# Optimization experiments

Hardware: AMD Instinct MI355X
Metric: run time of the kernel (lower is better)

## Reference

```python
import jax, jax.numpy as jnp
import numpy as np

N, E = 50000, 400000
D_NODE, D_EDGE = 128, 16
MSG_DIM, OUT_DIM = 128, 128
H_MSG, H_AGGR, H_UP = 256, 128, 256


def _dense(key, fin, fout):
    # xavier_uniform-scale gaussian init (exact distribution irrelevant for correctness)
    scale = jnp.sqrt(2.0 / (fin + fout)).astype(jnp.float32)
    w = jax.random.normal(key, (fin, fout), jnp.float32) * scale
    b = jnp.zeros((fout,), jnp.float32)
    return w, b


def setup_inputs() -> dict:
    key = jax.random.key(0)
    ks = jax.random.split(key, 13)
    nodes = jax.random.normal(ks[0], (N, D_NODE), jnp.float32)
    edges = jax.random.normal(ks[1], (E, D_EDGE), jnp.float32)
    senders = jax.random.randint(ks[2], (E,), 0, N, jnp.int32)
    receivers = jax.random.randint(ks[3], (E,), 0, N, jnp.int32)
    msg_in = D_EDGE + 2 * D_NODE
    msg_w1, msg_b1 = _dense(ks[4], msg_in, H_MSG)
    msg_w2, msg_b2 = _dense(ks[5], H_MSG, H_MSG)
    msg_w3, msg_b3 = _dense(ks[6], H_MSG, MSG_DIM)
    ag_w1, ag_b1 = _dense(ks[7], MSG_DIM, H_AGGR)
    ag_w2, ag_b2 = _dense(ks[8], H_AGGR, H_AGGR)
    ag_w3, ag_b3 = _dense(ks[9], H_AGGR, 1)
    up_w1, up_b1 = _dense(ks[10], D_NODE + MSG_DIM, H_UP)
    up_w2, up_b2 = _dense(ks[11], H_UP, H_UP)
    up_w3, up_b3 = _dense(ks[12], H_UP, OUT_DIM)
    return dict(nodes=nodes, edges=edges, senders=senders, receivers=receivers,
                msg_w1=msg_w1, msg_b1=msg_b1, msg_w2=msg_w2, msg_b2=msg_b2,
                msg_w3=msg_w3, msg_b3=msg_b3,
                ag_w1=ag_w1, ag_b1=ag_b1, ag_w2=ag_w2, ag_b2=ag_b2,
                ag_w3=ag_w3, ag_b3=ag_b3,
                up_w1=up_w1, up_b1=up_b1, up_w2=up_w2, up_b2=up_b2,
                up_w3=up_w3, up_b3=up_b3)


def reference(nodes, edges, senders, receivers,
              msg_w1, msg_b1, msg_w2, msg_b2, msg_w3, msg_b3,
              ag_w1, ag_b1, ag_w2, ag_b2, ag_w3, ag_b3,
              up_w1, up_b1, up_w2, up_b2, up_w3, up_b3):
    n = nodes.shape[0]
    # message_fn: concat(edge, sender, receiver) -> MLP(256,256) -> Dense(msg_dim)
    feats = jnp.concatenate([edges, nodes[senders], nodes[receivers]], axis=-1)  # [E, d_e+2d_n]
    h = jax.nn.relu(feats @ msg_w1 + msg_b1)      # relu after first hidden only (act_final=False)
    h = h @ msg_w2 + msg_b2
    msgs = h @ msg_w3 + msg_b3                    # [E, msg_dim]
    # aggregate_fn: gate MLP(128,128) -> Dense(1) -> segment_softmax over receivers
    g = jax.nn.relu(msgs @ ag_w1 + ag_b1)
    g = g @ ag_w2 + ag_b2
    gate = (g @ ag_w3 + ag_b3)[:, 0]              # [E]
    seg_max = jax.ops.segment_max(gate, receivers, num_segments=n)  # [N]
    w = jnp.exp(gate - seg_max[receivers])
    denom = jax.ops.segment_sum(w, receivers, num_segments=n)       # [N]
    attn = w / denom[receivers]                   # [E]
    aggr = jax.ops.segment_sum(attn[:, None] * msgs, receivers, num_segments=n)  # [N, msg_dim]
    # update_fn: concat(node, aggr) -> MLP(256,256) -> Dense(out_dim)
    u = jnp.concatenate([nodes, aggr], axis=-1)
    h = jax.nn.relu(u @ up_w1 + up_b1)
    h = h @ up_w2 + up_b2
    out = h @ up_w3 + up_b3                       # [N, out_dim]
    return out
```

## Files before the change

### kernel.cpp

```cpp
#include <hip/hip_runtime.h>
#include <stdint.h>


typedef _Float16 h16;
typedef _Float16 half8  __attribute__((ext_vector_type(8)));
typedef _Float16 h16x2  __attribute__((ext_vector_type(2)));
typedef float    f32x16 __attribute__((ext_vector_type(16)));
typedef unsigned u32x4  __attribute__((ext_vector_type(4)));

__device__ __forceinline__ f32x16 MFMA(half8 a, half8 b, f32x16 c) {
  return __builtin_amdgcn_mfma_f32_32x32x16_f16(a, b, c, 0, 0, 0);
}

__device__ __forceinline__ void lane_swap(unsigned &a, unsigned &b) {
  asm volatile("v_permlane32_swap_b32 %0, %1" : "+v"(a), "+v"(b));
}

__device__ __forceinline__ unsigned ordf(float f) {
  unsigned b = __float_as_uint(f);
  return (b & 0x80000000u) ? ~b : (b | 0x80000000u);
}
__device__ __forceinline__ float ordinv(unsigned u) {
  return __uint_as_float((u & 0x80000000u) ? (u ^ 0x80000000u) : ~u);
}

template<int MFA, int WAVES>
__device__ __forceinline__ void stage_tile(h16* dst, const h16* wT, int K, int kt, int tid) {
  int wv = tid >> 6, lane = tid & 63;
  static_assert((MFA * 2) % WAVES == 0, "tile chunks must divide evenly");
#pragma unroll
  for (int it = 0; it < (MFA * 2) / WAVES; ++it) {
    int slotbase = it * (WAVES * 64) + wv * 64;
    int s = slotbase + lane;
    int row = s >> 2, x = s & 3;
    int c = x ^ ((row >> 1) & 3);
    const h16* src = wT + (size_t)row * K + kt * 32 + c * 8;
    h16* d = dst + slotbase * 8;
    __builtin_amdgcn_global_load_lds((const __attribute__((address_space(1))) unsigned*)src,
                                     (__attribute__((address_space(3))) unsigned*)d, 16, 0, 0);
  }
}

__device__ __forceinline__ half8 ldsA(const h16* buf, int mf, int ksl, int lane) {
  int r31 = lane & 31, g = lane >> 5;
  int c = (2 * ksl + g) ^ ((r31 >> 1) & 3);
  return *(const half8*)(buf + mf * 1024 + r31 * 32 + c * 8);
}

template<bool RELU>
__device__ __forceinline__ void pack_frag(unsigned* hr, const f32x16 a, const float* bias, int g) {
#pragma unroll
  for (int j = 0; j < 8; ++j) {
    int m = 2 * (j & 1) + 8 * (j >> 1) + 4 * g;
    float x = a[2 * j]     + bias[m];
    float y = a[2 * j + 1] + bias[m + 1];
    if (RELU) { x = fmaxf(x, 0.f); y = fmaxf(y, 0.f); }
    auto p = __builtin_amdgcn_cvt_pkrtz(x, y);
    hr[j] = __builtin_bit_cast(unsigned, p);
  }
}

__device__ __forceinline__ half8 buildB(unsigned* hr, int ksl) {
  unsigned v0 = hr[4 * ksl + 0], v1 = hr[4 * ksl + 1];
  unsigned u0 = hr[4 * ksl + 2], u1 = hr[4 * ksl + 3];
  lane_swap(v0, u0);
  lane_swap(v1, u1);
  u32x4 t = {v0, v1, u0, u1};
  return __builtin_bit_cast(half8, t);
}

template<int MFA, int KT, int GB, int NMFA, int WAVES>
__device__ __forceinline__ void gemm_hregB(f32x16* acc, unsigned (*hreg)[8],
    const h16* wT, int K, const h16* nW, int nK,
    h16 (*wbuf)[8192], int tid, int lane) {
#pragma unroll
  for (int kt = 0; kt < KT; ++kt) {
    __syncthreads();
    if (kt + 1 < KT)  stage_tile<MFA, WAVES>(wbuf[(GB + kt + 1) & 1], wT, K, kt + 1, tid);
    else if (nW)      stage_tile<NMFA, WAVES>(wbuf[(GB + kt + 1) & 1], nW, nK, 0, tid);
    const h16* rb = wbuf[(GB + kt) & 1];
    __builtin_amdgcn_s_setprio(1);
#pragma unroll
    for (int ksl = 0; ksl < 2; ++ksl) {
      half8 b = buildB(hreg[kt], ksl);
#pragma unroll
      for (int mf = 0; mf < MFA; ++mf)
        acc[mf] = MFMA(ldsA(rb, mf, ksl, lane), b, acc[mf]);
    }
    __builtin_amdgcn_s_setprio(0);
  }
}

__global__ __launch_bounds__(256, 2) void k_edge(
    const h16* __restrict__ nodes_h, const h16* __restrict__ edges_h,
    const int* __restrict__ senders, const int* __restrict__ receivers,
    const int* __restrict__ perm,
    const h16* __restrict__ w1t, const h16* __restrict__ w2t, const h16* __restrict__ w3t,
    const h16* __restrict__ a1t, const h16* __restrict__ a2t,
    const float* __restrict__ b1, const float* __restrict__ b2, const float* __restrict__ b3,
    const float* __restrict__ ab1, const float* __restrict__ ab2,
    const float* __restrict__ ag3, const float* __restrict__ ab3,
    h16* __restrict__ msgs_h, float* __restrict__ gate, unsigned* __restrict__ segmax, int E)
{
  __shared__ h16 wbuf[2][8192];
  __shared__ float sb[1025];

  int tid = threadIdx.x, lane = tid & 63, wv = tid >> 6;
  int g = lane >> 5, c31 = lane & 31;

  sb[tid] = b1[tid];
  sb[256 + tid] = b2[tid];
  if (tid < 128) {
    sb[512 + tid] = b3[tid];
    sb[640 + tid] = ab1[tid];
    sb[768 + tid] = ab2[tid];
    sb[896 + tid] = ag3[tid];
  }
  if (tid == 0) sb[1024] = ab3[0];

  int e = blockIdx.x * 128 + wv * 32 + c31;
  bool ev = (e < E);
  int ec = ev ? e : (E - 1);
  int se = senders[ec], re = receivers[ec];
  int pidx = perm[ec];
  const h16* pe = edges_h + (size_t)ec * 16;
  const h16* ps = nodes_h + (size_t)se * 128;
  const h16* pr = nodes_h + (size_t)re * 128;

  stage_tile<8, 4>(wbuf[0], w1t, 288, 0, tid);

  auto loadB1 = [&](int ks) -> half8 {
    if (ks >= 17) { half8 z = {}; return z; }
    const h16* base = (ks == 0) ? pe : (ks < 9) ? (ps + 16 * ks - 16) : (pr + 16 * ks - 144);
    return *(const half8*)(base + 8 * g);
  };

  f32x16 acc1[8];
#pragma unroll
  for (int i = 0; i < 8; ++i) acc1[i] = f32x16{};
  half8 bq0 = loadB1(0), bq1 = loadB1(1);
#pragma unroll
  for (int kt = 0; kt < 9; ++kt) {
    __syncthreads();
    if (kt < 8) stage_tile<8, 4>(wbuf[(kt + 1) & 1], w1t, 288, kt + 1, tid);
    else        stage_tile<8, 4>(wbuf[1], w2t, 256, 0, tid);
    half8 n0 = {}, n1 = {};
    if (kt < 8) { n0 = loadB1(2 * kt + 2); n1 = loadB1(2 * kt + 3); }
    const h16* rb = wbuf[kt & 1];
    __builtin_amdgcn_s_setprio(1);
#pragma unroll
    for (int mf = 0; mf < 8; ++mf) acc1[mf] = MFMA(ldsA(rb, mf, 0, lane), bq0, acc1[mf]);
#pragma unroll
    for (int mf = 0; mf < 8; ++mf) acc1[mf] = MFMA(ldsA(rb, mf, 1, lane), bq1, acc1[mf]);
    __builtin_amdgcn_s_setprio(0);
    bq0 = n0; bq1 = n1;
  }
  unsigned hreg1[8][8];
#pragma unroll
  for (int mf = 0; mf < 8; ++mf) pack_frag<true>(hreg1[mf], acc1[mf], sb + 32 * mf, g);

  f32x16 acc2[8];
#pragma unroll
  for (int i = 0; i < 8; ++i) acc2[i] = f32x16{};
  gemm_hregB<8, 8, 9, 4, 4>(acc2, hreg1, w2t, 256, w3t, 256, wbuf, tid, lane);
  unsigned hreg2[8][8];
#pragma unroll
  for (int mf = 0; mf < 8; ++mf) pack_frag<false>(hreg2[mf], acc2[mf], sb + 256 + 32 * mf, g);

  f32x16 acc3[4];
#pragma unroll
  for (int i = 0; i < 4; ++i) acc3[i] = f32x16{};
  gemm_hregB<4, 8, 17, 4, 4>(acc3, hreg2, w3t, 256, a1t, 128, wbuf, tid, lane);
  unsigned hreg3[4][8];
  unsigned* mrow = (unsigned*)(msgs_h + (size_t)pidx * 128);
#pragma unroll
  for (int mf = 0; mf < 4; ++mf) {
    pack_frag<false>(hreg3[mf], acc3[mf], sb + 512 + 32 * mf, g);
    if (ev) {
#pragma unroll
      for (int j = 0; j < 8; ++j)
        mrow[16 * mf + (j & 1) + 4 * (j >> 1) + 2 * g] = hreg3[mf][j];
    }
  }

  f32x16 acc4[4];
#pragma unroll
  for (int i = 0; i < 4; ++i) acc4[i] = f32x16{};
  gemm_hregB<4, 4, 25, 4, 4>(acc4, hreg3, a1t, 128, a2t, 128, wbuf, tid, lane);
  unsigned hreg4[4][8];
#pragma unroll
  for (int mf = 0; mf < 4; ++mf) pack_frag<true>(hreg4[mf], acc4[mf], sb + 640 + 32 * mf, g);

  f32x16 acc5[4];
#pragma unroll
  for (int i = 0; i < 4; ++i) acc5[i] = f32x16{};
  gemm_hregB<4, 4, 29, 4, 4>(acc5, hreg4, a2t, 128, (const h16*)nullptr, 0, wbuf, tid, lane);

  float gs = 0.f;
#pragma unroll
  for (int mf = 0; mf < 4; ++mf)
#pragma unroll
    for (int r = 0; r < 16; ++r) {
      int m = 32 * mf + (r & 3) + 8 * (r >> 2) + 4 * g;
      gs += (acc5[mf][r] + sb[768 + m]) * sb[896 + m];
    }
  unsigned xa = __float_as_uint(gs), xb = xa;
  lane_swap(xa, xb);
  float tot = __uint_as_float(xa) + __uint_as_float(xb) + sb[1024];
  if (lane < 32 && ev) {
    gate[pidx] = tot;
    atomicMax(segmax + re, ordf(tot));
  }
}

__global__ __launch_bounds__(256, 2) void k_update(
    const h16* __restrict__ nodes_h, const h16* __restrict__ aggr_h,
    const h16* __restrict__ u1t, const h16* __restrict__ u2t, const h16* __restrict__ u3t,
    const float* __restrict__ b1, const float* __restrict__ b2, const float* __restrict__ b3,
    float* __restrict__ out, int N)
{
  __shared__ h16 wbuf[2][8192];
  __shared__ float sb[640];
  int tid = threadIdx.x, lane = tid & 63, wv = tid >> 6;
  int g = lane >> 5, c31 = lane & 31;
  sb[tid] = b1[tid];
  sb[256 + tid] = b2[tid];
  if (tid < 128) sb[512 + tid] = b3[tid];

  int n = blockIdx.x * 128 + wv * 32 + c31;
  int nc = (n < N) ? n : (N - 1);
  const h16* pn = nodes_h + (size_t)nc * 128;
  const h16* pa = aggr_h + (size_t)nc * 128;
  auto loadB = [&](int ks) -> half8 {
    const h16* base = (ks < 8) ? (pn + 16 * ks) : (pa + 16 * ks - 128);
    return *(const half8*)(base + 8 * g);
  };

  stage_tile<8, 4>(wbuf[0], u1t, 256, 0, tid);
  f32x16 acc1[8];
#pragma unroll
  for (int i = 0; i < 8; ++i) acc1[i] = f32x16{};
  half8 bq0 = loadB(0), bq1 = loadB(1);
#pragma unroll
  for (int kt = 0; kt < 8; ++kt) {
    __syncthreads();
    if (kt < 7) stage_tile<8, 4>(wbuf[(kt + 1) & 1], u1t, 256, kt + 1, tid);
    else        stage_tile<8, 4>(wbuf[0], u2t, 256, 0, tid);
    half8 n0 = {}, n1 = {};
    if (kt < 7) { n0 = loadB(2 * kt + 2); n1 = loadB(2 * kt + 3); }
    const h16* rb = wbuf[kt & 1];
    __builtin_amdgcn_s_setprio(1);
#pragma unroll
    for (int mf = 0; mf < 8; ++mf) acc1[mf] = MFMA(ldsA(rb, mf, 0, lane), bq0, acc1[mf]);
#pragma unroll
    for (int mf = 0; mf < 8; ++mf) acc1[mf] = MFMA(ldsA(rb, mf, 1, lane), bq1, acc1[mf]);
    __builtin_amdgcn_s_setprio(0);
    bq0 = n0; bq1 = n1;
  }
  unsigned hr1[8][8];
#pragma unroll
  for (int mf = 0; mf < 8; ++mf) pack_frag<true>(hr1[mf], acc1[mf], sb + 32 * mf, g);

  f32x16 acc2[8];
#pragma unroll
  for (int i = 0; i < 8; ++i) acc2[i] = f32x16{};
  gemm_hregB<8, 8, 8, 4, 4>(acc2, hr1, u2t, 256, u3t, 256, wbuf, tid, lane);
  unsigned hr2[8][8];
#pragma unroll
  for (int mf = 0; mf < 8; ++mf) pack_frag<false>(hr2[mf], acc2[mf], sb + 256 + 32 * mf, g);

  f32x16 acc3[4];
#pragma unroll
  for (int i = 0; i < 4; ++i) acc3[i] = f32x16{};
  gemm_hregB<4, 8, 16, 4, 4>(acc3, hr2, u3t, 256, (const h16*)nullptr, 0, wbuf, tid, lane);

  if (n < N) {
    float2* orow = (float2*)(out + (size_t)n * 128);
#pragma unroll
    for (int mf = 0; mf < 4; ++mf)
#pragma unroll
      for (int j = 0; j < 8; ++j) {
        int m = 32 * mf + 2 * (j & 1) + 8 * (j >> 1) + 4 * g;
        float2 v;
        v.x = acc3[mf][2 * j]     + sb[512 + m];
        v.y = acc3[mf][2 * j + 1] + sb[512 + m + 1];
        orow[m >> 1] = v;
      }
  }
}

struct WtArgs { const float* src[8]; h16* dst[8]; };

__global__ void k_prep_all(const float* __restrict__ nodes, const float* __restrict__ edges,
                           h16* __restrict__ nodes_h, h16* __restrict__ edges_h,
                           long n4n, long n4tot,
                           const int* __restrict__ recv, int* __restrict__ count, int E,
                           WtArgs a) {
  long i = (long)blockIdx.x * 256 + threadIdx.x;
  if (i < n4tot) {
    const float* src; h16* dst; long j;
    if (i < n4n) { src = nodes; dst = nodes_h; j = i; }
    else         { src = edges; dst = edges_h; j = i - n4n; }
    float4 v = ((const float4*)src)[j];
    union { h16 h[4]; uint2 u; } o;
    o.h[0] = (h16)v.x; o.h[1] = (h16)v.y; o.h[2] = (h16)v.z; o.h[3] = (h16)v.w;
    ((uint2*)dst)[j] = o.u;
  }
  if (i < E) atomicAdd(count + recv[i], 1);
  if (i < 368640) {
    int t = (int)i;
    constexpr int off[9] = {0, 73728, 139264, 172032, 188416, 204800, 270336, 335872, 368640};
    constexpr int Ks[8]  = {272, 256, 256, 128, 128, 256, 256, 256};
    constexpr int Os[8]  = {256, 256, 128, 128, 128, 256, 256, 128};
    constexpr int Kp[8]  = {288, 256, 256, 128, 128, 256, 256, 256};
#pragma unroll
    for (int sgi = 0; sgi < 8; ++sgi) {
      if (t >= off[sgi] && t < off[sgi + 1]) {
        int r = t - off[sgi];
        int o = r / Kp[sgi], k = r - o * Kp[sgi];
        a.dst[sgi][r] = (k < Ks[sgi]) ? (h16)a.src[sgi][(size_t)k * Os[sgi] + o] : (h16)0.f;
      }
    }
  }
}

__global__ __launch_bounds__(64) void k_scan(const int* __restrict__ count,
                                             int* __restrict__ starts,
                                             int* __restrict__ cursor, int N) {
  int lane = threadIdx.x;
  int total4 = (N + 3) >> 2;
  int chunk4 = (total4 + 63) >> 6;
  int lo4 = lane * chunk4;
  int hi4 = lo4 + chunk4;
  if (lo4 > total4) lo4 = total4;
  if (hi4 > total4) hi4 = total4;
  const int4* c4 = (const int4*)count;

  int s0 = 0, s1 = 0, s2 = 0, s3 = 0;
  int i = lo4;
  for (; i + 4 <= hi4; i += 4) {
    int4 v0 = c4[i], v1 = c4[i + 1], v2 = c4[i + 2], v3 = c4[i + 3];
    s0 += v0.x + v0.y + v0.z + v0.w;
    s1 += v1.x + v1.y + v1.z + v1.w;
    s2 += v2.x + v2.y + v2.z + v2.w;
    s3 += v3.x + v3.y + v3.z + v3.w;
  }
  for (; i < hi4; ++i) {
    int4 v = c4[i];
    s0 += v.x + v.y + v.z + v.w;
  }
  int sum = s0 + s1 + s2 + s3;

  int x = sum;
#pragma unroll
  for (int off = 1; off < 64; off <<= 1) {
    int t = __shfl_up(x, off, 64);
    if (lane >= off) x += t;
  }
  int run = x - sum;
  for (int j = lo4; j < hi4; ++j) {
    int4 v = c4[j];
    int4 s;
    s.x = run; run += v.x;
    s.y = run; run += v.y;
    s.z = run; run += v.z;
    s.w = run; run += v.w;
    ((int4*)starts)[j] = s;
    ((int4*)cursor)[j] = s;
  }
}

__global__ void k_fill(const int* __restrict__ recv, int* __restrict__ cursor,
                       int* __restrict__ perm, int E) {
  int e = blockIdx.x * 256 + threadIdx.x;
  if (e >= E) return;
  perm[e] = atomicAdd(cursor + recv[e], 1);
}

__global__ __launch_bounds__(256) void k_gather(
    const float* __restrict__ gate, const unsigned* __restrict__ segmax,
    const int* __restrict__ starts, const int* __restrict__ count,
    const h16* __restrict__ msgs_h, h16* __restrict__ aggr_h, int N)
{
  int node = (blockIdx.x * 256 + threadIdx.x) >> 6;
  int lane = threadIdx.x & 63;
  if (node >= N) return;
  int s = starts[node], c = count[node];
  float m = ordinv(segmax[node]);
  const unsigned* M = (const unsigned*)msgs_h;

  float den0 = 0.f, ax0 = 0.f, ay0 = 0.f;
  float den1 = 0.f, ax1 = 0.f, ay1 = 0.f;
  int i = 0;
  for (; i + 2 <= c; i += 2) {
    float w0 = __expf(gate[s + i]     - m);
    float w1 = __expf(gate[s + i + 1] - m);
    unsigned mv0 = M[(size_t)(s + i)     * 64 + lane];
    unsigned mv1 = M[(size_t)(s + i + 1) * 64 + lane];
    h16x2 h0 = __builtin_bit_cast(h16x2, mv0);
    h16x2 h1 = __builtin_bit_cast(h16x2, mv1);
    den0 += w0;                 den1 += w1;
    ax0 += w0 * (float)h0[0];   ax1 += w1 * (float)h1[0];
    ay0 += w0 * (float)h0[1];   ay1 += w1 * (float)h1[1];
  }
  if (i < c) {
    float w = __expf(gate[s + i] - m);
    unsigned mv = M[(size_t)(s + i) * 64 + lane];
    h16x2 hh = __builtin_bit_cast(h16x2, mv);
    den0 += w;
    ax0 += w * (float)hh[0];
    ay0 += w * (float)hh[1];
  }
  float den = den0 + den1, ax = ax0 + ax1, ay = ay0 + ay1;
  float inv = (c > 0) ? 1.f / den : 0.f;
  union { h16 h[2]; unsigned u; } o;
  o.h[0] = (h16)(ax * inv);
  o.h[1] = (h16)(ay * inv);
  ((unsigned*)aggr_h)[(size_t)node * 64 + lane] = o.u;
}

extern "C" void kernel_launch(void* const* d_in, const int* in_sizes, int n_in,
                              void* d_out, int out_size, void* d_ws, size_t ws_size,
                              hipStream_t stream) {
  const float* nodes  = (const float*)d_in[0];
  const float* edges  = (const float*)d_in[1];
  const int* senders  = (const int*)d_in[2];
  const int* receivers= (const int*)d_in[3];
  const float* msg_w1 = (const float*)d_in[4];  const float* msg_b1 = (const float*)d_in[5];
  const float* msg_w2 = (const float*)d_in[6];  const float* msg_b2 = (const float*)d_in[7];
  const float* msg_w3 = (const float*)d_in[8];  const float* msg_b3 = (const float*)d_in[9];
  const float* ag_w1  = (const float*)d_in[10]; const float* ag_b1  = (const float*)d_in[11];
  const float* ag_w2  = (const float*)d_in[12]; const float* ag_b2  = (const float*)d_in[13];
  const float* ag_w3  = (const float*)d_in[14]; const float* ag_b3  = (const float*)d_in[15];
  const float* up_w1  = (const float*)d_in[16]; const float* up_b1  = (const float*)d_in[17];
  const float* up_w2  = (const float*)d_in[18]; const float* up_b2  = (const float*)d_in[19];
  const float* up_w3  = (const float*)d_in[20]; const float* up_b3  = (const float*)d_in[21];

  int N = in_sizes[0] / 128;
  int E = in_sizes[2];
  float* out = (float*)d_out;

  char* ws = (char*)d_ws;
  size_t off = 0;
  auto alloc = [&](size_t bytes) -> char* {
    char* p = ws + off; off += (bytes + 255) & ~(size_t)255; return p;
  };
  h16* nodes_h = (h16*)alloc((size_t)N * 128 * 2);
  h16* edges_h = (h16*)alloc((size_t)E * 16 * 2);
  h16* w1t = (h16*)alloc(256 * 288 * 2);
  h16* w2t = (h16*)alloc(256 * 256 * 2);
  h16* w3t = (h16*)alloc(128 * 256 * 2);
  h16* a1t = (h16*)alloc(128 * 128 * 2);
  h16* a2t = (h16*)alloc(128 * 128 * 2);
  h16* u1t = (h16*)alloc(256 * 256 * 2);
  h16* u2t = (h16*)alloc(256 * 256 * 2);
  h16* u3t = (h16*)alloc(128 * 256 * 2);
  h16* msgs_h = (h16*)alloc((size_t)E * 128 * 2);
  float* gate = (float*)alloc((size_t)E * 4);
  unsigned* segmax = (unsigned*)alloc((size_t)N * 8 + 16);
  int* count  = (int*)(segmax + N);
  int* starts = (int*)alloc((size_t)N * 4 + 16);
  int* cursor = (int*)alloc((size_t)N * 4 + 16);
  int* perm   = (int*)alloc((size_t)E * 4);
  h16* aggr_h = (h16*)alloc((size_t)N * 128 * 2);

  hipMemsetAsync(segmax, 0, (size_t)N * 8 + 16, stream);

  WtArgs wa;
  wa.src[0] = msg_w1; wa.dst[0] = w1t;
  wa.src[1] = msg_w2; wa.dst[1] = w2t;
  wa.src[2] = msg_w3; wa.dst[2] = w3t;
  wa.src[3] = ag_w1;  wa.dst[3] = a1t;
  wa.src[4] = ag_w2;  wa.dst[4] = a2t;
  wa.src[5] = up_w1;  wa.dst[5] = u1t;
  wa.src[6] = up_w2;  wa.dst[6] = u2t;
  wa.src[7] = up_w3;  wa.dst[7] = u3t;

  long n4n = (long)N * 128 / 4, n4e = (long)E * 16 / 4;
  long n4tot = n4n + n4e;
  long gmax = n4tot;
  k_prep_all<<<(int)((gmax + 255) / 256), 256, 0, stream>>>(
      nodes, edges, nodes_h, edges_h, n4n, n4tot, receivers, count, E, wa);

  k_scan<<<1, 64, 0, stream>>>(count, starts, cursor, N);
  k_fill<<<(E + 255) / 256, 256, 0, stream>>>(receivers, cursor, perm, E);

  k_edge<<<(E + 127) / 128, 256, 0, stream>>>(
      nodes_h, edges_h, senders, receivers, perm, w1t, w2t, w3t, a1t, a2t,
      msg_b1, msg_b2, msg_b3, ag_b1, ag_b2, ag_w3, ag_b3,
      msgs_h, gate, segmax, E);

  k_gather<<<(int)(((size_t)N * 64 + 255) / 256), 256, 0, stream>>>(
      gate, segmax, starts, count, msgs_h, aggr_h, N);

  k_update<<<(N + 127) / 128, 256, 0, stream>>>(
      nodes_h, aggr_h, u1t, u2t, u3t, up_b1, up_b2, up_b3, out, N);
}
```

Baseline: 365.4 us.

## Stage two weight tiles per barrier with a four-buffer LDS ring

Shared weight staging moves from a double buffer to a four-slot ring, and each iteration stages and consumes two K-tiles per __syncthreads. This halves the number of barriers in every GEMM stage of the edge and update kernels. The first-layer weight is padded from K=288 to 320 so its tile count becomes even. LDS use per block doubles to about 64KB for the buffers, which may cut occupancy below two blocks per CU. More B fragments are also kept in registers, adding register pressure.

```diff
diff --git a/kernel.cpp b/kernel.cpp
--- a/kernel.cpp
+++ b/kernel.cpp
@@ -70,22 +70,32 @@
 }
 
 template<int MFA, int KT, int GB, int NMFA, int WAVES>
-__device__ __forceinline__ void gemm_hregB(f32x16* acc, unsigned (*hreg)[8],
+__device__ __forceinline__ void gemm_hregB2(f32x16* acc, unsigned (*hreg)[8],
     const h16* wT, int K, const h16* nW, int nK,
     h16 (*wbuf)[8192], int tid, int lane) {
-#pragma unroll
-  for (int kt = 0; kt < KT; ++kt) {
+  static_assert(KT % 2 == 0, "KT must be even");
+#pragma unroll
+  for (int q = 0; q < KT / 2; ++q) {
     __syncthreads();
-    if (kt + 1 < KT)  stage_tile<MFA, WAVES>(wbuf[(GB + kt + 1) & 1], wT, K, kt + 1, tid);
-    else if (nW)      stage_tile<NMFA, WAVES>(wbuf[(GB + kt + 1) & 1], nW, nK, 0, tid);
-    const h16* rb = wbuf[(GB + kt) & 1];
+    if (2 * q + 2 < KT) {
+      stage_tile<MFA, WAVES>(wbuf[(GB + 2 * q + 2) & 3], wT, K, 2 * q + 2, tid);
+      stage_tile<MFA, WAVES>(wbuf[(GB + 2 * q + 3) & 3], wT, K, 2 * q + 3, tid);
+    } else if (nW) {
+      stage_tile<NMFA, WAVES>(wbuf[(GB + KT) & 3], nW, nK, 0, tid);
+      stage_tile<NMFA, WAVES>(wbuf[(GB + KT + 1) & 3], nW, nK, 1, tid);
+    }
     __builtin_amdgcn_s_setprio(1);
 #pragma unroll
-    for (int ksl = 0; ksl < 2; ++ksl) {
-      half8 b = buildB(hreg[kt], ksl);
-#pragma unroll
-      for (int mf = 0; mf < MFA; ++mf)
-        acc[mf] = MFMA(ldsA(rb, mf, ksl, lane), b, acc[mf]);
+    for (int tt = 0; tt < 2; ++tt) {
+      int t = 2 * q + tt;
+      const h16* rb = wbuf[(GB + t) & 3];
+#pragma unroll
+      for (int ksl = 0; ksl < 2; ++ksl) {
+        half8 b = buildB(hreg[t], ksl);
+#pragma unroll
+        for (int mf = 0; mf < MFA; ++mf)
+          acc[mf] = MFMA(ldsA(rb, mf, ksl, lane), b, acc[mf]);
+      }
     }
     __builtin_amdgcn_s_setprio(0);
   }
@@ -102,7 +112,7 @@
     const float* __restrict__ ag3, const float* __restrict__ ab3,
     h16* __restrict__ msgs_h, float* __restrict__ gate, unsigned* __restrict__ segmax, int E)
 {
-  __shared__ h16 wbuf[2][8192];
+  __shared__ h16 wbuf[4][8192];
   __shared__ float sb[1025];
 
   int tid = threadIdx.x, lane = tid & 63, wv = tid >> 6;
@@ -127,7 +137,8 @@
   const h16* ps = nodes_h + (size_t)se * 128;
   const h16* pr = nodes_h + (size_t)re * 128;
 
-  stage_tile<8, 4>(wbuf[0], w1t, 288, 0, tid);
+  stage_tile<8, 4>(wbuf[0], w1t, 320, 0, tid);
+  stage_tile<8, 4>(wbuf[1], w1t, 320, 1, tid);
 
   auto loadB1 = [&](int ks) -> half8 {
     if (ks >= 17) { half8 z = {}; return z; }
@@ -138,22 +149,36 @@
   f32x16 acc1[8];
 #pragma unroll
   for (int i = 0; i < 8; ++i) acc1[i] = f32x16{};
-  half8 bq0 = loadB1(0), bq1 = loadB1(1);
-#pragma unroll
-  for (int kt = 0; kt < 9; ++kt) {
+  half8 bq[4], bn[4];
+#pragma unroll
+  for (int s = 0; s < 4; ++s) bq[s] = loadB1(s);
+#pragma unroll
+  for (int q = 0; q < 5; ++q) {
     __syncthreads();
-    if (kt < 8) stage_tile<8, 4>(wbuf[(kt + 1) & 1], w1t, 288, kt + 1, tid);
-    else        stage_tile<8, 4>(wbuf[1], w2t, 256, 0, tid);
-    half8 n0 = {}, n1 = {};
-    if (kt < 8) { n0 = loadB1(2 * kt + 2); n1 = loadB1(2 * kt + 3); }
-    const h16* rb = wbuf[kt & 1];
+    if (q < 4) {
+      stage_tile<8, 4>(wbuf[(2 * q + 2) & 3], w1t, 320, 2 * q + 2, tid);
+      stage_tile<8, 4>(wbuf[(2 * q + 3) & 3], w1t, 320, 2 * q + 3, tid);
+#pragma unroll
+      for (int s = 0; s < 4; ++s) bn[s] = loadB1(4 * q + 4 + s);
+    } else {
+      stage_tile<8, 4>(wbuf[2], w2t, 256, 0, tid);
+      stage_tile<8, 4>(wbuf[3], w2t, 256, 1, tid);
+    }
     __builtin_amdgcn_s_setprio(1);
 #pragma unroll
-    for (int mf = 0; mf < 8; ++mf) acc1[mf] = MFMA(ldsA(rb, mf, 0, lane), bq0, acc1[mf]);
-#pragma unroll
-    for (int mf = 0; mf < 8; ++mf) acc1[mf] = MFMA(ldsA(rb, mf, 1, lane), bq1, acc1[mf]);
+    for (int tt = 0; tt < 2; ++tt) {
+      const h16* rb = wbuf[(2 * q + tt) & 3];
+#pragma unroll
+      for (int ksl = 0; ksl < 2; ++ksl) {
+        half8 b = bq[2 * tt + ksl];
+#pragma unroll
+        for (int mf = 0; mf < 8; ++mf)
+          acc1[mf] = MFMA(ldsA(rb, mf, ksl, lane), b, acc1[mf]);
+      }
+    }
     __builtin_amdgcn_s_setprio(0);
-    bq0 = n0; bq1 = n1;
+#pragma unroll
+    for (int s = 0; s < 4; ++s) bq[s] = bn[s];
   }
   unsigned hreg1[8][8];
 #pragma unroll
@@ -162,7 +187,7 @@
   f32x16 acc2[8];
 #pragma unroll
   for (int i = 0; i < 8; ++i) acc2[i] = f32x16{};
-  gemm_hregB<8, 8, 9, 4, 4>(acc2, hreg1, w2t, 256, w3t, 256, wbuf, tid, lane);
+  gemm_hregB2<8, 8, 10, 4, 4>(acc2, hreg1, w2t, 256, w3t, 256, wbuf, tid, lane);
   unsigned hreg2[8][8];
 #pragma unroll
   for (int mf = 0; mf < 8; ++mf) pack_frag<false>(hreg2[mf], acc2[mf], sb + 256 + 32 * mf, g);
@@ -170,7 +195,7 @@
   f32x16 acc3[4];
 #pragma unroll
   for (int i = 0; i < 4; ++i) acc3[i] = f32x16{};
-  gemm_hregB<4, 8, 17, 4, 4>(acc3, hreg2, w3t, 256, a1t, 128, wbuf, tid, lane);
+  gemm_hregB2<4, 8, 18, 4, 4>(acc3, hreg2, w3t, 256, a1t, 128, wbuf, tid, lane);
   unsigned hreg3[4][8];
   unsigned* mrow = (unsigned*)(msgs_h + (size_t)pidx * 128);
 #pragma unroll
@@ -186,7 +211,7 @@
   f32x16 acc4[4];
 #pragma unroll
   for (int i = 0; i < 4; ++i) acc4[i] = f32x16{};
-  gemm_hregB<4, 4, 25, 4, 4>(acc4, hreg3, a1t, 128, a2t, 128, wbuf, tid, lane);
+  gemm_hregB2<4, 4, 26, 4, 4>(acc4, hreg3, a1t, 128, a2t, 128, wbuf, tid, lane);
   unsigned hreg4[4][8];
 #pragma unroll
   for (int mf = 0; mf < 4; ++mf) pack_frag<true>(hreg4[mf], acc4[mf], sb + 640 + 32 * mf, g);
@@ -194,7 +219,7 @@
   f32x16 acc5[4];
 #pragma unroll
   for (int i = 0; i < 4; ++i) acc5[i] = f32x16{};
-  gemm_hregB<4, 4, 29, 4, 4>(acc5, hreg4, a2t, 128, (const h16*)nullptr, 0, wbuf, tid, lane);
+  gemm_hregB2<4, 4, 30, 4, 4>(acc5, hreg4, a2t, 128, (const h16*)nullptr, 0, wbuf, tid, lane);
 
   float gs = 0.f;
 #pragma unroll
@@ -219,7 +244,7 @@
     const float* __restrict__ b1, const float* __restrict__ b2, const float* __restrict__ b3,
     float* __restrict__ out, int N)
 {
-  __shared__ h16 wbuf[2][8192];
+  __shared__ h16 wbuf[4][8192];
   __shared__ float sb[640];
   int tid = threadIdx.x, lane = tid & 63, wv = tid >> 6;
   int g = lane >> 5, c31 = lane & 31;
@@ -237,25 +262,41 @@
   };
 
   stage_tile<8, 4>(wbuf[0], u1t, 256, 0, tid);
+  stage_tile<8, 4>(wbuf[1], u1t, 256, 1, tid);
+
   f32x16 acc1[8];
 #pragma unroll
   for (int i = 0; i < 8; ++i) acc1[i] = f32x16{};
-  half8 bq0 = loadB(0), bq1 = loadB(1);
-#pragma unroll
-  for (int kt = 0; kt < 8; ++kt) {
+  half8 bq[4], bn[4];
+#pragma unroll
+  for (int s = 0; s < 4; ++s) bq[s] = loadB(s);
+#pragma unroll
+  for (int q = 0; q < 4; ++q) {
     __syncthreads();
-    if (kt < 7) stage_tile<8, 4>(wbuf[(kt + 1) & 1], u1t, 256, kt + 1, tid);
-    else        stage_tile<8, 4>(wbuf[0], u2t, 256, 0, tid);
-    half8 n0 = {}, n1 = {};
-    if (kt < 7) { n0 = loadB(2 * kt + 2); n1 = loadB(2 * kt + 3); }
-    const h16* rb = wbuf[kt & 1];
+    if (q < 3) {
+      stage_tile<8, 4>(wbuf[(2 * q + 2) & 3], u1t, 256, 2 * q + 2, tid);
+      stage_tile<8, 4>(wbuf[(2 * q + 3) & 3], u1t, 256, 2 * q + 3, tid);
+#pragma unroll
+      for (int s = 0; s < 4; ++s) bn[s] = loadB(4 * q + 4 + s);
+    } else {
+      stage_tile<8, 4>(wbuf[0], u2t, 256, 0, tid);
+      stage_tile<8, 4>(wbuf[1], u2t, 256, 1, tid);
+    }
     __builtin_amdgcn_s_setprio(1);
 #pragma unroll
-    for (int mf = 0; mf < 8; ++mf) acc1[mf] = MFMA(ldsA(rb, mf, 0, lane), bq0, acc1[mf]);
-#pragma unroll
-    for (int mf = 0; mf < 8; ++mf) acc1[mf] = MFMA(ldsA(rb, mf, 1, lane), bq1, acc1[mf]);
+    for (int tt = 0; tt < 2; ++tt) {
+      const h16* rb = wbuf[(2 * q + tt) & 3];
+#pragma unroll
+      for (int ksl = 0; ksl < 2; ++ksl) {
+        half8 b = bq[2 * tt + ksl];
+#pragma unroll
+        for (int mf = 0; mf < 8; ++mf)
+          acc1[mf] = MFMA(ldsA(rb, mf, ksl, lane), b, acc1[mf]);
+      }
+    }
     __builtin_amdgcn_s_setprio(0);
-    bq0 = n0; bq1 = n1;
+#pragma unroll
+    for (int s = 0; s < 4; ++s) bq[s] = bn[s];
   }
   unsigned hr1[8][8];
 #pragma unroll
@@ -264,7 +305,7 @@
   f32x16 acc2[8];
 #pragma unroll
   for (int i = 0; i < 8; ++i) acc2[i] = f32x16{};
-  gemm_hregB<8, 8, 8, 4, 4>(acc2, hr1, u2t, 256, u3t, 256, wbuf, tid, lane);
+  gemm_hregB2<8, 8, 8, 4, 4>(acc2, hr1, u2t, 256, u3t, 256, wbuf, tid, lane);
   unsigned hr2[8][8];
 #pragma unroll
   for (int mf = 0; mf < 8; ++mf) pack_frag<false>(hr2[mf], acc2[mf], sb + 256 + 32 * mf, g);
@@ -272,7 +313,7 @@
   f32x16 acc3[4];
 #pragma unroll
   for (int i = 0; i < 4; ++i) acc3[i] = f32x16{};
-  gemm_hregB<4, 8, 16, 4, 4>(acc3, hr2, u3t, 256, (const h16*)nullptr, 0, wbuf, tid, lane);
+  gemm_hregB2<4, 8, 16, 4, 4>(acc3, hr2, u3t, 256, (const h16*)nullptr, 0, wbuf, tid, lane);
 
   if (n < N) {
     float2* orow = (float2*)(out + (size_t)n * 128);
@@ -307,12 +348,12 @@
     ((uint2*)dst)[j] = o.u;
   }
   if (i < E) atomicAdd(count + recv[i], 1);
-  if (i < 368640) {
+  if (i < 376832) {
     int t = (int)i;
-    constexpr int off[9] = {0, 73728, 139264, 172032, 188416, 204800, 270336, 335872, 368640};
+    constexpr int off[9] = {0, 81920, 147456, 180224, 196608, 212992, 278528, 344064, 376832};
     constexpr int Ks[8]  = {272, 256, 256, 128, 128, 256, 256, 256};
     constexpr int Os[8]  = {256, 256, 128, 128, 128, 256, 256, 128};
-    constexpr int Kp[8]  = {288, 256, 256, 128, 128, 256, 256, 256};
+    constexpr int Kp[8]  = {320, 256, 256, 128, 128, 256, 256, 256};
 #pragma unroll
     for (int sgi = 0; sgi < 8; ++sgi) {
       if (t >= off[sgi] && t < off[sgi + 1]) {
@@ -447,7 +488,7 @@
   };
   h16* nodes_h = (h16*)alloc((size_t)N * 128 * 2);
   h16* edges_h = (h16*)alloc((size_t)E * 16 * 2);
-  h16* w1t = (h16*)alloc(256 * 288 * 2);
+  h16* w1t = (h16*)alloc(256 * 320 * 2);
   h16* w2t = (h16*)alloc(256 * 256 * 2);
   h16* w3t = (h16*)alloc(128 * 256 * 2);
   h16* a1t = (h16*)alloc(128 * 128 * 2);
```

Measured after the change: 363.1 us. Within noise of the previous version (-0.6%).

## Triple-buffer weight tiles with vmcnt-based sync and fuse receiver ranking into prep

Applied to the files above, without the earlier changes.

The weight staging in the edge and update kernels moves from a two-buffer ring to a three-buffer ring with prefetch distance two. The per-step __syncthreads is replaced by a partial s_waitcnt vmcnt plus s_barrier, so loads for the next tile can stay in flight during compute. Separately, the per-edge rank within its receiver segment is taken from the counting atomic in the prep kernel, which removes the cursor copy and the k_fill kernel; the edge kernel then computes its sorted slot as starts[re]+rank. The extra 16KB of LDS per block may limit occupancy, and the hand-tuned vmcnt counts must match the exact number of loads each wave has issued.

```diff
diff --git a/kernel.cpp b/kernel.cpp
--- a/kernel.cpp
+++ b/kernel.cpp
@@ -22,6 +22,17 @@
 }
 __device__ __forceinline__ float ordinv(unsigned u) {
   return __uint_as_float((u & 0x80000000u) ? (u ^ 0x80000000u) : ~u);
+}
+
+template<int N>
+__device__ __forceinline__ void phase_sync() {
+  if constexpr (N >= 8)      asm volatile("s_waitcnt vmcnt(8)" ::: "memory");
+  else if constexpr (N == 6) asm volatile("s_waitcnt vmcnt(6)" ::: "memory");
+  else if constexpr (N == 4) asm volatile("s_waitcnt vmcnt(4)" ::: "memory");
+  else if constexpr (N == 2) asm volatile("s_waitcnt vmcnt(2)" ::: "memory");
+  else                       asm volatile("s_waitcnt vmcnt(0)" ::: "memory");
+  __builtin_amdgcn_sched_barrier(0);
+  __builtin_amdgcn_s_barrier();
 }
 
 template<int MFA, int WAVES>
@@ -70,31 +81,35 @@
 }
 
 template<int MFA, int KT, int GB, int NMFA, int WAVES>
-__device__ __forceinline__ void gemm_hregB(f32x16* acc, unsigned (*hreg)[8],
+__device__ __forceinline__ void gemm_hregB3(f32x16* acc, unsigned (*hreg)[8],
     const h16* wT, int K, const h16* nW, int nK,
     h16 (*wbuf)[8192], int tid, int lane) {
 #pragma unroll
-  for (int kt = 0; kt < KT; ++kt) {
-    __syncthreads();
-    if (kt + 1 < KT)  stage_tile<MFA, WAVES>(wbuf[(GB + kt + 1) & 1], wT, K, kt + 1, tid);
-    else if (nW)      stage_tile<NMFA, WAVES>(wbuf[(GB + kt + 1) & 1], nW, nK, 0, tid);
-    const h16* rb = wbuf[(GB + kt) & 1];
+  for (int t = 0; t < KT; ++t) {
+    if (t + 2 < KT)
+      stage_tile<MFA, WAVES>(wbuf[(GB + t + 2) % 3], wT, K, t + 2, tid);
+    else if (nW != nullptr)
+      stage_tile<NMFA, WAVES>(wbuf[(GB + t + 2) % 3], nW, nK, t + 2 - KT, tid);
+    const h16* rb = wbuf[(GB + t) % 3];
     __builtin_amdgcn_s_setprio(1);
 #pragma unroll
     for (int ksl = 0; ksl < 2; ++ksl) {
-      half8 b = buildB(hreg[kt], ksl);
+      half8 b = buildB(hreg[t], ksl);
 #pragma unroll
       for (int mf = 0; mf < MFA; ++mf)
         acc[mf] = MFMA(ldsA(rb, mf, ksl, lane), b, acc[mf]);
     }
     __builtin_amdgcn_s_setprio(0);
+    if (t + 2 < KT)          phase_sync<MFA / 2>();
+    else if (nW != nullptr)  phase_sync<NMFA / 2>();
+    else                     phase_sync<0>();
   }
 }
 
 __global__ __launch_bounds__(256, 2) void k_edge(
     const h16* __restrict__ nodes_h, const h16* __restrict__ edges_h,
     const int* __restrict__ senders, const int* __restrict__ receivers,
-    const int* __restrict__ perm,
+    const int* __restrict__ starts, const int* __restrict__ rank,
     const h16* __restrict__ w1t, const h16* __restrict__ w2t, const h16* __restrict__ w3t,
     const h16* __restrict__ a1t, const h16* __restrict__ a2t,
     const float* __restrict__ b1, const float* __restrict__ b2, const float* __restrict__ b3,
@@ -102,7 +117,7 @@
     const float* __restrict__ ag3, const float* __restrict__ ab3,
     h16* __restrict__ msgs_h, float* __restrict__ gate, unsigned* __restrict__ segmax, int E)
 {
-  __shared__ h16 wbuf[2][8192];
+  __shared__ h16 wbuf[3][8192];
   __shared__ float sb[1025];
 
   int tid = threadIdx.x, lane = tid & 63, wv = tid >> 6;
@@ -122,12 +137,10 @@
   bool ev = (e < E);
   int ec = ev ? e : (E - 1);
   int se = senders[ec], re = receivers[ec];
-  int pidx = perm[ec];
+  int pidx = starts[re] + rank[ec];
   const h16* pe = edges_h + (size_t)ec * 16;
   const h16* ps = nodes_h + (size_t)se * 128;
   const h16* pr = nodes_h + (size_t)re * 128;
-
-  stage_tile<8, 4>(wbuf[0], w1t, 288, 0, tid);
 
   auto loadB1 = [&](int ks) -> half8 {
     if (ks >= 17) { half8 z = {}; return z; }
@@ -135,25 +148,35 @@
     return *(const half8*)(base + 8 * g);
   };
 
+  stage_tile<8, 4>(wbuf[0], w1t, 288, 0, tid);
+  stage_tile<8, 4>(wbuf[1], w1t, 288, 1, tid);
+  half8 bq0 = loadB1(0), bq1 = loadB1(1);
+  half8 bm0 = loadB1(2), bm1 = loadB1(3);
+  half8 bn0 = {}, bn1 = {};
+  phase_sync<8>();
+
   f32x16 acc1[8];
 #pragma unroll
   for (int i = 0; i < 8; ++i) acc1[i] = f32x16{};
-  half8 bq0 = loadB1(0), bq1 = loadB1(1);
-#pragma unroll
-  for (int kt = 0; kt < 9; ++kt) {
-    __syncthreads();
-    if (kt < 8) stage_tile<8, 4>(wbuf[(kt + 1) & 1], w1t, 288, kt + 1, tid);
-    else        stage_tile<8, 4>(wbuf[1], w2t, 256, 0, tid);
-    half8 n0 = {}, n1 = {};
-    if (kt < 8) { n0 = loadB1(2 * kt + 2); n1 = loadB1(2 * kt + 3); }
-    const h16* rb = wbuf[kt & 1];
+#pragma unroll
+  for (int t = 0; t < 9; ++t) {
+    if (t + 2 < 9) {
+      stage_tile<8, 4>(wbuf[(t + 2) % 3], w1t, 288, t + 2, tid);
+      bn0 = loadB1(2 * t + 4);
+      bn1 = loadB1(2 * t + 5);
+    } else {
+      stage_tile<8, 4>(wbuf[(t + 2) % 3], w2t, 256, t - 7, tid);
+    }
+    const h16* rb = wbuf[t % 3];
     __builtin_amdgcn_s_setprio(1);
 #pragma unroll
     for (int mf = 0; mf < 8; ++mf) acc1[mf] = MFMA(ldsA(rb, mf, 0, lane), bq0, acc1[mf]);
 #pragma unroll
     for (int mf = 0; mf < 8; ++mf) acc1[mf] = MFMA(ldsA(rb, mf, 1, lane), bq1, acc1[mf]);
     __builtin_amdgcn_s_setprio(0);
-    bq0 = n0; bq1 = n1;
+    bq0 = bm0; bq1 = bm1; bm0 = bn0; bm1 = bn1;
+    if (t + 2 < 9) phase_sync<6>();
+    else           phase_sync<4>();
   }
   unsigned hreg1[8][8];
 #pragma unroll
@@ -162,7 +185,7 @@
   f32x16 acc2[8];
 #pragma unroll
   for (int i = 0; i < 8; ++i) acc2[i] = f32x16{};
-  gemm_hregB<8, 8, 9, 4, 4>(acc2, hreg1, w2t, 256, w3t, 256, wbuf, tid, lane);
+  gemm_hregB3<8, 8, 9, 4, 4>(acc2, hreg1, w2t, 256, w3t, 256, wbuf, tid, lane);
   unsigned hreg2[8][8];
 #pragma unroll
   for (int mf = 0; mf < 8; ++mf) pack_frag<false>(hreg2[mf], acc2[mf], sb + 256 + 32 * mf, g);
@@ -170,7 +193,7 @@
   f32x16 acc3[4];
 #pragma unroll
   for (int i = 0; i < 4; ++i) acc3[i] = f32x16{};
-  gemm_hregB<4, 8, 17, 4, 4>(acc3, hreg2, w3t, 256, a1t, 128, wbuf, tid, lane);
+  gemm_hregB3<4, 8, 17, 4, 4>(acc3, hreg2, w3t, 256, a1t, 128, wbuf, tid, lane);
   unsigned hreg3[4][8];
   unsigned* mrow = (unsigned*)(msgs_h + (size_t)pidx * 128);
 #pragma unroll
@@ -186,7 +209,7 @@
   f32x16 acc4[4];
 #pragma unroll
   for (int i = 0; i < 4; ++i) acc4[i] = f32x16{};
-  gemm_hregB<4, 4, 25, 4, 4>(acc4, hreg3, a1t, 128, a2t, 128, wbuf, tid, lane);
+  gemm_hregB3<4, 4, 25, 4, 4>(acc4, hreg3, a1t, 128, a2t, 128, wbuf, tid, lane);
   unsigned hreg4[4][8];
 #pragma unroll
   for (int mf = 0; mf < 4; ++mf) pack_frag<true>(hreg4[mf], acc4[mf], sb + 640 + 32 * mf, g);
@@ -194,7 +217,7 @@
   f32x16 acc5[4];
 #pragma unroll
   for (int i = 0; i < 4; ++i) acc5[i] = f32x16{};
-  gemm_hregB<4, 4, 29, 4, 4>(acc5, hreg4, a2t, 128, (const h16*)nullptr, 0, wbuf, tid, lane);
+  gemm_hregB3<4, 4, 29, 4, 4>(acc5, hreg4, a2t, 128, (const h16*)nullptr, 0, wbuf, tid, lane);
 
   float gs = 0.f;
 #pragma unroll
@@ -219,7 +242,7 @@
     const float* __restrict__ b1, const float* __restrict__ b2, const float* __restrict__ b3,
     float* __restrict__ out, int N)
 {
-  __shared__ h16 wbuf[2][8192];
+  __shared__ h16 wbuf[3][8192];
   __shared__ float sb[640];
   int tid = threadIdx.x, lane = tid & 63, wv = tid >> 6;
   int g = lane >> 5, c31 = lane & 31;
@@ -237,25 +260,34 @@
   };
 
   stage_tile<8, 4>(wbuf[0], u1t, 256, 0, tid);
+  stage_tile<8, 4>(wbuf[1], u1t, 256, 1, tid);
+  half8 bq0 = loadB(0), bq1 = loadB(1);
+  half8 bm0 = loadB(2), bm1 = loadB(3);
+  half8 bn0 = {}, bn1 = {};
+  phase_sync<8>();
+
   f32x16 acc1[8];
 #pragma unroll
   for (int i = 0; i < 8; ++i) acc1[i] = f32x16{};
-  half8 bq0 = loadB(0), bq1 = loadB(1);
-#pragma unroll
-  for (int kt = 0; kt < 8; ++kt) {
-    __syncthreads();
-    if (kt < 7) stage_tile<8, 4>(wbuf[(kt + 1) & 1], u1t, 256, kt + 1, tid);
-    else        stage_tile<8, 4>(wbuf[0], u2t, 256, 0, tid);
-    half8 n0 = {}, n1 = {};
-    if (kt < 7) { n0 = loadB(2 * kt + 2); n1 = loadB(2 * kt + 3); }
-    const h16* rb = wbuf[kt & 1];
+#pragma unroll
+  for (int t = 0; t < 8; ++t) {
+    if (t + 2 < 8) {
+      stage_tile<8, 4>(wbuf[(t + 2) % 3], u1t, 256, t + 2, tid);
+      bn0 = loadB(2 * t + 4);
+      bn1 = loadB(2 * t + 5);
+    } else {
+      stage_tile<8, 4>(wbuf[(t + 2) % 3], u2t, 256, t - 6, tid);
+    }
+    const h16* rb = wbuf[t % 3];
     __builtin_amdgcn_s_setprio(1);
 #pragma unroll
     for (int mf = 0; mf < 8; ++mf) acc1[mf] = MFMA(ldsA(rb, mf, 0, lane), bq0, acc1[mf]);
 #pragma unroll
     for (int mf = 0; mf < 8; ++mf) acc1[mf] = MFMA(ldsA(rb, mf, 1, lane), bq1, acc1[mf]);
     __builtin_amdgcn_s_setprio(0);
-    bq0 = n0; bq1 = n1;
+    bq0 = bm0; bq1 = bm1; bm0 = bn0; bm1 = bn1;
+    if (t + 2 < 8) phase_sync<6>();
+    else           phase_sync<4>();
   }
   unsigned hr1[8][8];
 #pragma unroll
@@ -264,7 +296,7 @@
   f32x16 acc2[8];
 #pragma unroll
   for (int i = 0; i < 8; ++i) acc2[i] = f32x16{};
-  gemm_hregB<8, 8, 8, 4, 4>(acc2, hr1, u2t, 256, u3t, 256, wbuf, tid, lane);
+  gemm_hregB3<8, 8, 8, 4, 4>(acc2, hr1, u2t, 256, u3t, 256, wbuf, tid, lane);
   unsigned hr2[8][8];
 #pragma unroll
   for (int mf = 0; mf < 8; ++mf) pack_frag<false>(hr2[mf], acc2[mf], sb + 256 + 32 * mf, g);
@@ -272,7 +304,7 @@
   f32x16 acc3[4];
 #pragma unroll
   for (int i = 0; i < 4; ++i) acc3[i] = f32x16{};
-  gemm_hregB<4, 8, 16, 4, 4>(acc3, hr2, u3t, 256, (const h16*)nullptr, 0, wbuf, tid, lane);
+  gemm_hregB3<4, 8, 16, 4, 4>(acc3, hr2, u3t, 256, (const h16*)nullptr, 0, wbuf, tid, lane);
 
   if (n < N) {
     float2* orow = (float2*)(out + (size_t)n * 128);
@@ -294,7 +326,8 @@
 __global__ void k_prep_all(const float* __restrict__ nodes, const float* __restrict__ edges,
                            h16* __restrict__ nodes_h, h16* __restrict__ edges_h,
                            long n4n, long n4tot,
-                           const int* __restrict__ recv, int* __restrict__ count, int E,
+                           const int* __restrict__ recv, int* __restrict__ count,
+                           int* __restrict__ rank, int E,
                            WtArgs a) {
   long i = (long)blockIdx.x * 256 + threadIdx.x;
   if (i < n4tot) {
@@ -306,7 +339,7 @@
     o.h[0] = (h16)v.x; o.h[1] = (h16)v.y; o.h[2] = (h16)v.z; o.h[3] = (h16)v.w;
     ((uint2*)dst)[j] = o.u;
   }
-  if (i < E) atomicAdd(count + recv[i], 1);
+  if (i < E) rank[i] = atomicAdd(count + recv[i], 1);
   if (i < 368640) {
     int t = (int)i;
     constexpr int off[9] = {0, 73728, 139264, 172032, 188416, 204800, 270336, 335872, 368640};
@@ -325,8 +358,7 @@
 }
 
 __global__ __launch_bounds__(64) void k_scan(const int* __restrict__ count,
-                                             int* __restrict__ starts,
-                                             int* __restrict__ cursor, int N) {
+                                             int* __restrict__ starts, int N) {
   int lane = threadIdx.x;
   int total4 = (N + 3) >> 2;
   int chunk4 = (total4 + 63) >> 6;
@@ -366,15 +398,7 @@
     s.z = run; run += v.z;
     s.w = run; run += v.w;
     ((int4*)starts)[j] = s;
-    ((int4*)cursor)[j] = s;
-  }
-}
-
-__global__ void k_fill(const int* __restrict__ recv, int* __restrict__ cursor,
-                       int* __restrict__ perm, int E) {
-  int e = blockIdx.x * 256 + threadIdx.x;
-  if (e >= E) return;
-  perm[e] = atomicAdd(cursor + recv[e], 1);
+  }
 }
 
 __global__ __launch_bounds__(256) void k_gather(
@@ -460,8 +484,7 @@
   unsigned* segmax = (unsigned*)alloc((size_t)N * 8 + 16);
   int* count  = (int*)(segmax + N);
   int* starts = (int*)alloc((size_t)N * 4 + 16);
-  int* cursor = (int*)alloc((size_t)N * 4 + 16);
-  int* perm   = (int*)alloc((size_t)E * 4);
+  int* rank   = (int*)alloc((size_t)E * 4);
   h16* aggr_h = (h16*)alloc((size_t)N * 128 * 2);
 
   hipMemsetAsync(segmax, 0, (size_t)N * 8 + 16, stream);
@@ -480,13 +503,12 @@
   long n4tot = n4n + n4e;
   long gmax = n4tot;
   k_prep_all<<<(int)((gmax + 255) / 256), 256, 0, stream>>>(
-      nodes, edges, nodes_h, edges_h, n4n, n4tot, receivers, count, E, wa);
-
-  k_scan<<<1, 64, 0, stream>>>(count, starts, cursor, N);
-  k_fill<<<(E + 255) / 256, 256, 0, stream>>>(receivers, cursor, perm, E);
+      nodes, edges, nodes_h, edges_h, n4n, n4tot, receivers, count, rank, E, wa);
+
+  k_scan<<<1, 64, 0, stream>>>(count, starts, N);
 
   k_edge<<<(E + 127) / 128, 256, 0, stream>>>(
-      nodes_h, edges_h, senders, receivers, perm, w1t, w2t, w3t, a1t, a2t,
+      nodes_h, edges_h, senders, receivers, starts, rank, w1t, w2t, w3t, a1t, a2t,
       msg_b1, msg_b2, msg_b3, ag_b1, ag_b2, ag_w3, ag_b3,
       msgs_h, gate, segmax, E);
 
```

New measurement: 363.5 us. Within noise of the previous version (-0.5%).
